# Performance work log

Hardware: AMD Instinct MI355X
Metric: run time of the kernel (lower is better)

Reference implementation:

```python
import jax, jax.numpy as jnp
import numpy as np

B, W, H, C = 8, 32, 32, 64   # batch, width, height, hidden_size
NH = 8                        # num_attention_heads
M = 32                        # max_position_embeddings
P = C // 2                    # position_embedding_size (query_positional_score=True)


def setup_inputs() -> dict:
    key = jax.random.key(0)
    ks = jax.random.split(key, 7)
    s = 0.02
    return {
        "hidden_states": jax.random.normal(ks[0], (B, W, H, C), dtype=jnp.float32),
        "row_emb": jax.random.normal(ks[1], (2 * M - 1, P), dtype=jnp.float32) * s,
        "col_emb": jax.random.normal(ks[2], (2 * M - 1, P), dtype=jnp.float32) * s,
        "Wq": jax.random.normal(ks[3], (NH * C, C), dtype=jnp.float32) * s,
        "bq": jnp.zeros((NH * C,), dtype=jnp.float32),
        "Wk": jax.random.normal(ks[4], (NH * C, C), dtype=jnp.float32) * s,
        "bk": jnp.zeros((NH * C,), dtype=jnp.float32),
        "Wv": jax.random.normal(ks[5], (C, NH * C), dtype=jnp.float32) * s,
        "bv": jnp.zeros((C,), dtype=jnp.float32),
    }


def reference(hidden_states, row_emb, col_emb, Wq, bq, Wk, bk, Wv, bv):
    b, w, h, c = hidden_states.shape
    nh = Wq.shape[0] // c
    half = c // 2
    center = row_emb.shape[0] // 2  # = max_position_embeddings - 1

    # projections: all_head_size = nh * c (per source: hidden_size * num_heads)
    q = (hidden_states @ Wq.T + bq).reshape(b, w, h, nh, c)
    k = (hidden_states @ Wk.T + bk).reshape(b, w, h, nh, c)

    # relative index tables: rel[i, j] = (j - i) + (M - 1)
    iw = jnp.arange(w)
    ih = jnp.arange(h)
    rel_w = iw[None, :] - iw[:, None] + center   # (w, w)
    rel_h = ih[None, :] - ih[:, None] + center   # (h, h)
    r_emb = row_emb[rel_w]  # (w, w, P)
    c_emb = col_emb[rel_h]  # (h, h, P)

    # positional scores: q split into row/col halves
    q_row = q[..., :half]
    q_col = q[..., half:]
    row_scores = jnp.einsum('bijhd,ikd->bijhk', q_row, r_emb)  # (b,w,h,nh,w)
    col_scores = jnp.einsum('bijhd,jld->bijhl', q_col, c_emb)  # (b,w,h,nh,h)
    scale = jnp.sqrt(jnp.asarray(c, dtype=hidden_states.dtype))
    scores = (row_scores[..., :, None] + col_scores[..., None, :]) / scale  # (b,w,h,nh,w,h)

    # content scores q^T k
    scores = scores + jnp.einsum('bijhd,bklhd->bijhkl', q, k) / scale

    # softmax over merged spatial key dims (k,l)
    probs = jax.nn.softmax(scores.reshape(b, w, h, nh, w * h), axis=-1).reshape(scores.shape)

    # value mixing directly with hidden_states, then output projection
    mixed = jnp.einsum('bijhkl,bkld->bijhd', probs, hidden_states).reshape(b, w, h, nh * c)
    return mixed @ Wv.T + bv
```

## Files before the change

### kernel.cpp

```cpp
#include <hip/hip_runtime.h>
#include <math.h>

typedef __bf16 bf16;
typedef bf16 bf16x2 __attribute__((ext_vector_type(2)));
typedef bf16 bf16x4 __attribute__((ext_vector_type(4)));
typedef bf16 bf16x8 __attribute__((ext_vector_type(8)));
typedef float f32x4 __attribute__((ext_vector_type(4)));

constexpr int CENTER = 31;
constexpr float QSCALE = 0.125f * 1.4426950408889634f;

static __device__ __forceinline__ unsigned short f2bf_bits(float f) {
    bf16 b = (bf16)f;
    return __builtin_bit_cast(unsigned short, b);
}

static __device__ __forceinline__ float fast_exp2(float x) {
#if __has_builtin(__builtin_amdgcn_exp2f)
    return __builtin_amdgcn_exp2f(x);
#else
    return exp2f(x);
#endif
}

__global__ __launch_bounds__(256)
void prep_kernel(const float* __restrict__ hid,
                 const float* __restrict__ Wq, const float* __restrict__ Wk,
                 const float* __restrict__ Wv,
                 bf16* __restrict__ hb, bf16* __restrict__ htb,
                 bf16* __restrict__ Wqb, bf16* __restrict__ Wkb,
                 bf16* __restrict__ Wvp)
{
    __shared__ __attribute__((aligned(16))) bf16 hs[64][72];

    const int t   = threadIdx.x;
    const int blk = blockIdx.x;
    const int b   = blk >> 4, kc = blk & 15;

    {
        int row = t >> 2, c4 = (t & 3) * 16;
        const float4* src = (const float4*)(hid + ((size_t)b * 1024 + kc * 64 + row) * 64 + c4);
        bf16 tmp[16];
        #pragma unroll
        for (int u = 0; u < 4; ++u) {
            float4 v = src[u];
            tmp[4*u+0] = (bf16)v.x; tmp[4*u+1] = (bf16)v.y;
            tmp[4*u+2] = (bf16)v.z; tmp[4*u+3] = (bf16)v.w;
        }
        *(int4*)&hs[row][c4]     = ((int4*)tmp)[0];
        *(int4*)&hs[row][c4 + 8] = ((int4*)tmp)[1];
        bf16* hdst = hb + ((size_t)b * 1024 + kc * 64 + row) * 64 + c4;
        *(int4*)hdst       = ((int4*)tmp)[0];
        *(int4*)(hdst + 8) = ((int4*)tmp)[1];
    }

    {
        int idx = blk * 256 + t;
        if (idx < 8192) {
            float4 vq = ((const float4*)Wq)[idx];
            float4 vk = ((const float4*)Wk)[idx];
            float4 vv = ((const float4*)Wv)[idx];
            ushort4 pq, pk2, pv;
            pq.x = f2bf_bits(vq.x); pq.y = f2bf_bits(vq.y); pq.z = f2bf_bits(vq.z); pq.w = f2bf_bits(vq.w);
            pk2.x = f2bf_bits(vk.x); pk2.y = f2bf_bits(vk.y); pk2.z = f2bf_bits(vk.z); pk2.w = f2bf_bits(vk.w);
            pv.x = f2bf_bits(vv.x); pv.y = f2bf_bits(vv.y); pv.z = f2bf_bits(vv.z); pv.w = f2bf_bits(vv.w);
            ((ushort4*)Wqb)[idx] = pq;
            ((ushort4*)Wkb)[idx] = pk2;
            int c = idx >> 7, o4 = (idx & 127) * 4;
            size_t dst = (size_t)((c >> 4) * 16 + (o4 >> 5)) * 512 + (c & 15) * 32 + (o4 & 31);
            *(ushort4*)(Wvp + dst) = pv;
        }
    }
    __syncthreads();

    {
        int d = t >> 2, p0 = (t & 3) * 16;
        ushort tmp[16];
        #pragma unroll
        for (int i = 0; i < 16; ++i)
            tmp[i] = __builtin_bit_cast(unsigned short, hs[p0 + i][d]);
        bf16* dst = htb + ((size_t)b * 64 + d) * 1024 + kc * 64 + p0;
        *(int4*)dst       = ((int4*)tmp)[0];
        *(int4*)(dst + 8) = ((int4*)tmp)[1];
    }
}

__global__ __launch_bounds__(256)
void qkproj_kernel(const bf16* __restrict__ hb,
                   const bf16* __restrict__ Wqb, const float* __restrict__ bq,
                   const bf16* __restrict__ Wkb, const float* __restrict__ bk,
                   bf16* __restrict__ qb, bf16* __restrict__ kb)
{
    __shared__ __attribute__((aligned(16))) bf16 As[128][72];
    __shared__ __attribute__((aligned(16))) bf16 Bs[128][72];

    const int t  = threadIdx.x;
    const int pt = blockIdx.x;
    const int ot = blockIdx.y;
    const int z  = blockIdx.z;
    const int p0 = pt * 128;
    const int b  = p0 >> 10;

    const bf16* Wb        = z ? Wkb : Wqb;
    const float* bias     = z ? bk : bq;
    bf16* outp            = z ? kb : qb;
    const float scale     = z ? 1.0f : QSCALE;

    {
        int row = t >> 1, ch = (t & 1) * 32;
        const int4* asrc = (const int4*)(hb + (size_t)(p0 + row) * 64 + ch);
        const int4* bsrc = (const int4*)(Wb + (size_t)(ot * 128 + row) * 64 + ch);
        #pragma unroll
        for (int u = 0; u < 4; ++u) {
            *(int4*)&As[row][ch + u * 8] = asrc[u];
            *(int4*)&Bs[row][ch + u * 8] = bsrc[u];
        }
    }
    __syncthreads();

    const int w = t >> 6, ln = t & 63, l15 = ln & 15, quad = ln >> 4;

    bf16x8 a[2][2];
    #pragma unroll
    for (int mt = 0; mt < 2; ++mt) {
        a[mt][0] = *(const bf16x8*)&As[w * 32 + mt * 16 + l15][quad * 8];
        a[mt][1] = *(const bf16x8*)&As[w * 32 + mt * 16 + l15][32 + quad * 8];
    }

    const f32x4 z4 = {0.f, 0.f, 0.f, 0.f};
    f32x4 acc[2][8];
    #pragma unroll
    for (int mt = 0; mt < 2; ++mt)
        #pragma unroll
        for (int nt = 0; nt < 8; ++nt) acc[mt][nt] = z4;

    #pragma unroll
    for (int nt = 0; nt < 8; ++nt) {
        bf16x8 b0 = *(const bf16x8*)&Bs[nt * 16 + l15][quad * 8];
        bf16x8 b1 = *(const bf16x8*)&Bs[nt * 16 + l15][32 + quad * 8];
        #pragma unroll
        for (int mt = 0; mt < 2; ++mt) {
            acc[mt][nt] = __builtin_amdgcn_mfma_f32_16x16x32_bf16(a[mt][0], b0, acc[mt][nt], 0, 0, 0);
            acc[mt][nt] = __builtin_amdgcn_mfma_f32_16x16x32_bf16(a[mt][1], b1, acc[mt][nt], 0, 0, 0);
        }
    }

    #pragma unroll
    for (int nt = 0; nt < 8; ++nt) {
        int o = ot * 128 + nt * 16 + l15;
        float bv = bias[o];
        int hh = o >> 6, d = o & 63;
        #pragma unroll
        for (int mt = 0; mt < 2; ++mt)
            #pragma unroll
            for (int r = 0; r < 4; ++r) {
                int pos = (p0 & 1023) + w * 32 + mt * 16 + quad * 4 + r;
                float val = (acc[mt][nt][r] + bv) * scale;
                outp[(((size_t)b * 8 + hh) * 1024 + pos) * 64 + d] = (bf16)val;
            }
    }
}

__global__ __launch_bounds__(256)
void bias_kernel(const bf16* __restrict__ qb,
                 const float* __restrict__ row_emb, const float* __restrict__ col_emb,
                 bf16* __restrict__ rowbias, bf16* __restrict__ colbias)
{
    __shared__ __attribute__((aligned(16))) bf16 embRs[63][40];
    __shared__ __attribute__((aligned(16))) bf16 embCs[63][40];

    const int t  = threadIdx.x;
    const int bh = blockIdx.x;
    const int sg = blockIdx.y;

    for (int i = t; i < 2016; i += 256) embRs[i >> 5][i & 31] = (bf16)row_emb[i];
    for (int i = t; i < 2016; i += 256) embCs[i >> 5][i & 31] = (bf16)col_emb[i];
    __syncthreads();

    const int w = t >> 6, ln = t & 63, l15 = ln & 15, quad = ln >> 4;

    #pragma unroll
    for (int u = 0; u < 2; ++u) {
        int s = sg * 8 + u * 4 + w;
        bool cm = s >= 32;
        int ij = cm ? s - 32 : s;

        bf16x8 a[2];
        #pragma unroll
        for (int mt = 0; mt < 2; ++mt) {
            const bf16* ap = cm
                ? qb + ((size_t)bh * 1024 + (mt * 16 + l15) * 32 + ij) * 64 + 32 + quad * 8
                : qb + ((size_t)bh * 1024 + ij * 32 + mt * 16 + l15) * 64 + quad * 8;
            a[mt] = *(const bf16x8*)ap;
        }
        bf16* ob = cm ? colbias : rowbias;

        #pragma unroll
        for (int nt = 0; nt < 2; ++nt) {
            int erow = nt * 16 + l15 + CENTER - ij;
            bf16x8 bfrag = cm ? *(const bf16x8*)&embCs[erow][quad * 8]
                              : *(const bf16x8*)&embRs[erow][quad * 8];
            #pragma unroll
            for (int mt = 0; mt < 2; ++mt) {
                f32x4 c = {0.f, 0.f, 0.f, 0.f};
                c = __builtin_amdgcn_mfma_f32_16x16x32_bf16(a[mt], bfrag, c, 0, 0, 0);
                #pragma unroll
                for (int r = 0; r < 4; ++r) {
                    int ql = mt * 16 + quad * 4 + r;
                    int qrow = cm ? ql * 32 + ij : ij * 32 + ql;
                    ob[((size_t)bh * 1024 + qrow) * 32 + nt * 16 + l15] = (bf16)c[r];
                }
            }
        }
    }
}

__global__ __launch_bounds__(256, 2)
void attn_kernel(const bf16* __restrict__ qb, const bf16* __restrict__ kb,
                 const bf16* __restrict__ htb,
                 const bf16* __restrict__ rowbias, const bf16* __restrict__ colbias,
                 bf16* __restrict__ mixedb)
{
    __shared__ __attribute__((aligned(16))) bf16 Ks[64][72];
    __shared__ __attribute__((aligned(16))) bf16 Hts[64][72];
    __shared__ __attribute__((aligned(16))) bf16 Pp[4][32][72];

    const int t  = threadIdx.x;
    const int id = blockIdx.x;
    const int r8 = id & 7;
    const int g  = id >> 3;
    const int qt = g & 7;
    const int bh = r8 * 8 + (g >> 3);
    const int b  = bh >> 3, h = bh & 7;
    const int q0 = qt * 128;
    const int w = t >> 6, ln = t & 63, l15 = ln & 15, quad = ln >> 4;

    bf16x8 bq_[2][2];
    float  cbv[2][2][4];
    const bf16* rbp[2];
    #pragma unroll
    for (int mt = 0; mt < 2; ++mt) {
        int qrow = q0 + w * 32 + mt * 16 + l15;
        const bf16* qp = qb + ((size_t)bh * 1024 + qrow) * 64;
        bq_[mt][0] = *(const bf16x8*)(qp + quad * 8);
        bq_[mt][1] = *(const bf16x8*)(qp + 32 + quad * 8);
        #pragma unroll
        for (int par = 0; par < 2; ++par) {
            bf16x4 cv = *(const bf16x4*)(colbias + ((size_t)bh * 1024 + qrow) * 32 + par * 16 + quad * 4);
            #pragma unroll
            for (int r = 0; r < 4; ++r) cbv[mt][par][r] = (float)cv[r];
        }
        rbp[mt] = rowbias + ((size_t)bh * 1024 + qrow) * 32;
    }

    const f32x4 z4 = {0.f, 0.f, 0.f, 0.f};
    f32x4 oacc[2][4];
    float lsum[2] = {0.f, 0.f};
    #pragma unroll
    for (int mt = 0; mt < 2; ++mt)
        #pragma unroll
        for (int dt = 0; dt < 4; ++dt) oacc[mt][dt] = z4;

    bf16* Pw = &Pp[w][0][0];
    const bf16* kcbase = kb + (size_t)bh * 1024 * 64;
    const bf16* hcbase = htb + (size_t)b * 64 * 1024;

    const int srow = t >> 2, sc = (t & 3) << 4;
    const bf16* kptr = kcbase + (size_t)srow * 64 + sc;
    const bf16* hptr = hcbase + (size_t)srow * 1024 + sc;

    int4 kr0 = *(const int4*)(kptr);
    int4 kr1 = *(const int4*)(kptr + 8);
    int4 hr0 = *(const int4*)(hptr);
    int4 hr1 = *(const int4*)(hptr + 8);
    bf16x2 rnext[2];
    #pragma unroll
    for (int mt = 0; mt < 2; ++mt) rnext[mt] = *(const bf16x2*)(rbp[mt]);

    for (int kc = 0; kc < 16; ++kc) {
        __syncthreads();
        *(int4*)&Ks[srow][sc]      = kr0;
        *(int4*)&Ks[srow][sc + 8]  = kr1;
        *(int4*)&Hts[srow][sc]     = hr0;
        *(int4*)&Hts[srow][sc + 8] = hr1;
        float rb[2][2];
        #pragma unroll
        for (int mt = 0; mt < 2; ++mt) {
            rb[mt][0] = (float)rnext[mt][0];
            rb[mt][1] = (float)rnext[mt][1];
        }
        __syncthreads();

        if (kc < 15) {
            const bf16* kn = kptr + (size_t)(kc + 1) * 4096;
            const bf16* hn = hptr + (size_t)(kc + 1) * 64;
            kr0 = *(const int4*)(kn);
            kr1 = *(const int4*)(kn + 8);
            hr0 = *(const int4*)(hn);
            hr1 = *(const int4*)(hn + 8);
            #pragma unroll
            for (int mt = 0; mt < 2; ++mt)
                rnext[mt] = *(const bf16x2*)(rbp[mt] + (kc + 1) * 2);
        }

        f32x4 sf[2][4];
        #pragma unroll
        for (int mt = 0; mt < 2; ++mt)
            #pragma unroll
            for (int kt = 0; kt < 4; ++kt) sf[mt][kt] = z4;
        __builtin_amdgcn_s_setprio(1);
        #pragma unroll
        for (int kt = 0; kt < 4; ++kt) {
            bf16x8 aK0 = *(const bf16x8*)&Ks[kt * 16 + l15][quad * 8];
            bf16x8 aK1 = *(const bf16x8*)&Ks[kt * 16 + l15][32 + quad * 8];
            #pragma unroll
            for (int mt = 0; mt < 2; ++mt) {
                sf[mt][kt] = __builtin_amdgcn_mfma_f32_16x16x32_bf16(aK0, bq_[mt][0], sf[mt][kt], 0, 0, 0);
                sf[mt][kt] = __builtin_amdgcn_mfma_f32_16x16x32_bf16(aK1, bq_[mt][1], sf[mt][kt], 0, 0, 0);
            }
        }
        __builtin_amdgcn_s_setprio(0);

        #pragma unroll
        for (int mt = 0; mt < 2; ++mt)
            #pragma unroll
            for (int kt = 0; kt < 4; ++kt) {
                float rbv = rb[mt][kt >> 1];
                ushort4 pk;
                float p0 = fast_exp2(sf[mt][kt][0] + rbv + cbv[mt][kt & 1][0]);
                float p1 = fast_exp2(sf[mt][kt][1] + rbv + cbv[mt][kt & 1][1]);
                float p2 = fast_exp2(sf[mt][kt][2] + rbv + cbv[mt][kt & 1][2]);
                float p3 = fast_exp2(sf[mt][kt][3] + rbv + cbv[mt][kt & 1][3]);
                lsum[mt] += (p0 + p1) + (p2 + p3);
                pk.x = f2bf_bits(p0); pk.y = f2bf_bits(p1);
                pk.z = f2bf_bits(p2); pk.w = f2bf_bits(p3);
                *(ushort4*)&Pw[(mt * 16 + l15) * 72 + kt * 16 + quad * 4] = pk;
            }

        bf16x8 bp[2][2];
        #pragma unroll
        for (int mt = 0; mt < 2; ++mt) {
            bp[mt][0] = *(const bf16x8*)&Pw[(mt * 16 + l15) * 72 + quad * 8];
            bp[mt][1] = *(const bf16x8*)&Pw[(mt * 16 + l15) * 72 + 32 + quad * 8];
        }
        __builtin_amdgcn_s_setprio(1);
        #pragma unroll
        for (int dt = 0; dt < 4; ++dt) {
            bf16x8 aH0 = *(const bf16x8*)&Hts[dt * 16 + l15][quad * 8];
            bf16x8 aH1 = *(const bf16x8*)&Hts[dt * 16 + l15][32 + quad * 8];
            #pragma unroll
            for (int mt = 0; mt < 2; ++mt) {
                oacc[mt][dt] = __builtin_amdgcn_mfma_f32_16x16x32_bf16(aH0, bp[mt][0], oacc[mt][dt], 0, 0, 0);
                oacc[mt][dt] = __builtin_amdgcn_mfma_f32_16x16x32_bf16(aH1, bp[mt][1], oacc[mt][dt], 0, 0, 0);
            }
        }
        __builtin_amdgcn_s_setprio(0);
    }

    float inv[2];
    #pragma unroll
    for (int mt = 0; mt < 2; ++mt) {
        float v = lsum[mt];
        v += __shfl_xor(v, 16);
        v += __shfl_xor(v, 32);
        inv[mt] = 1.0f / v;
    }
    #pragma unroll
    for (int mt = 0; mt < 2; ++mt) {
        int pos = q0 + w * 32 + mt * 16 + l15;
        bf16* mb = mixedb + ((size_t)b * 1024 + pos) * 512 + h * 64;
        #pragma unroll
        for (int dt = 0; dt < 4; ++dt) {
            ushort4 pk;
            pk.x = f2bf_bits(oacc[mt][dt][0] * inv[mt]);
            pk.y = f2bf_bits(oacc[mt][dt][1] * inv[mt]);
            pk.z = f2bf_bits(oacc[mt][dt][2] * inv[mt]);
            pk.w = f2bf_bits(oacc[mt][dt][3] * inv[mt]);
            *(ushort4*)(mb + dt * 16 + quad * 4) = pk;
        }
    }
}

__global__ __launch_bounds__(256)
void out_proj_kernel(const bf16* __restrict__ mixedb,
                     const bf16* __restrict__ Wvp, const float* __restrict__ bv,
                     float* __restrict__ out)
{
    const int t  = threadIdx.x;
    const int p0 = blockIdx.x * 16;
    const int w = t >> 6, ln = t & 63, l15 = ln & 15, quad = ln >> 4;

    float bvv = bv[w * 16 + l15];
    f32x4 acc = {bvv, bvv, bvv, bvv};

    const bf16* arow  = mixedb + (size_t)(p0 + l15) * 512 + quad * 8;
    const bf16* bbase = Wvp + (size_t)w * 16 * 512 + l15 * 32 + quad * 8;

    #pragma unroll
    for (int kc = 0; kc < 16; ++kc) {
        bf16x8 a0 = *(const bf16x8*)(arow + kc * 32);
        bf16x8 bfrag = *(const bf16x8*)(bbase + kc * 512);
        acc = __builtin_amdgcn_mfma_f32_16x16x32_bf16(a0, bfrag, acc, 0, 0, 0);
    }

    #pragma unroll
    for (int r = 0; r < 4; ++r)
        out[(size_t)(p0 + quad * 4 + r) * 64 + w * 16 + l15] = acc[r];
}

extern "C" void kernel_launch(void* const* d_in, const int* in_sizes, int n_in,
                              void* d_out, int out_size, void* d_ws, size_t ws_size,
                              hipStream_t stream)
{
    const float* hid     = (const float*)d_in[0];
    const float* row_emb = (const float*)d_in[1];
    const float* col_emb = (const float*)d_in[2];
    const float* Wq      = (const float*)d_in[3];
    const float* bq      = (const float*)d_in[4];
    const float* Wk      = (const float*)d_in[5];
    const float* bk      = (const float*)d_in[6];
    const float* Wv      = (const float*)d_in[7];
    const float* bv      = (const float*)d_in[8];
    float* out = (float*)d_out;

    bf16* qb      = (bf16*)d_ws;
    bf16* kb      = qb + (size_t)64 * 1024 * 64;
    bf16* htb     = kb + (size_t)64 * 1024 * 64;
    bf16* rowbias = htb + (size_t)8 * 64 * 1024;
    bf16* colbias = rowbias + (size_t)64 * 1024 * 32;
    bf16* mixedb  = colbias + (size_t)64 * 1024 * 32;
    bf16* hb      = mixedb + (size_t)8 * 1024 * 512;
    bf16* Wqb     = hb + (size_t)8 * 1024 * 64;
    bf16* Wkb     = Wqb + (size_t)512 * 64;
    bf16* Wvp     = Wkb + (size_t)512 * 64;

    prep_kernel<<<128, 256, 0, stream>>>(hid, Wq, Wk, Wv, hb, htb, Wqb, Wkb, Wvp);
    qkproj_kernel<<<dim3(64, 4, 2), 256, 0, stream>>>(hb, Wqb, bq, Wkb, bk, qb, kb);
    bias_kernel<<<dim3(64, 8), 256, 0, stream>>>(qb, row_emb, col_emb, rowbias, colbias);
    attn_kernel<<<512, 256, 0, stream>>>(qb, kb, htb, rowbias, colbias, mixedb);
    out_proj_kernel<<<512, 256, 0, stream>>>(mixedb, Wvp, bv, out);
}
```

Measured before the change: 133.3 us.

## Double-buffer K/H tiles in attention and process two row tiles per out-proj block

The attention kernel now keeps two shared-memory buffers for the K and hidden-state tiles. Global loads are prefetched two chunks ahead and the next tile is written into the spare buffer, so each iteration needs one barrier instead of two. The output projection kernel now computes 32 rows per block, reusing each weight fragment for two MFMAs, and launches half as many blocks. The attention kernel's shared memory grows, which could limit occupancy.

```diff
diff --git a/kernel.cpp b/kernel.cpp
--- a/kernel.cpp
+++ b/kernel.cpp
@@ -221,8 +221,8 @@
                  const bf16* __restrict__ rowbias, const bf16* __restrict__ colbias,
                  bf16* __restrict__ mixedb)
 {
-    __shared__ __attribute__((aligned(16))) bf16 Ks[64][72];
-    __shared__ __attribute__((aligned(16))) bf16 Hts[64][72];
+    __shared__ __attribute__((aligned(16))) bf16 Ks[2][64][72];
+    __shared__ __attribute__((aligned(16))) bf16 Hts[2][64][72];
     __shared__ __attribute__((aligned(16))) bf16 Pp[4][32][72];
 
     const int t  = threadIdx.x;
@@ -273,36 +273,49 @@
     int4 kr1 = *(const int4*)(kptr + 8);
     int4 hr0 = *(const int4*)(hptr);
     int4 hr1 = *(const int4*)(hptr + 8);
+    *(int4*)&Ks[0][srow][sc]       = kr0;
+    *(int4*)&Ks[0][srow][sc + 8]   = kr1;
+    *(int4*)&Hts[0][srow][sc]      = hr0;
+    *(int4*)&Hts[0][srow][sc + 8]  = hr1;
+    kr0 = *(const int4*)(kptr + 4096);
+    kr1 = *(const int4*)(kptr + 4096 + 8);
+    hr0 = *(const int4*)(hptr + 64);
+    hr1 = *(const int4*)(hptr + 64 + 8);
     bf16x2 rnext[2];
     #pragma unroll
     for (int mt = 0; mt < 2; ++mt) rnext[mt] = *(const bf16x2*)(rbp[mt]);
-
+    __syncthreads();
+
+    int cur = 0;
     for (int kc = 0; kc < 16; ++kc) {
-        __syncthreads();
-        *(int4*)&Ks[srow][sc]      = kr0;
-        *(int4*)&Ks[srow][sc + 8]  = kr1;
-        *(int4*)&Hts[srow][sc]     = hr0;
-        *(int4*)&Hts[srow][sc + 8] = hr1;
+        if (kc < 15) {
+            *(int4*)&Ks[cur ^ 1][srow][sc]      = kr0;
+            *(int4*)&Ks[cur ^ 1][srow][sc + 8]  = kr1;
+            *(int4*)&Hts[cur ^ 1][srow][sc]     = hr0;
+            *(int4*)&Hts[cur ^ 1][srow][sc + 8] = hr1;
+        }
         float rb[2][2];
         #pragma unroll
         for (int mt = 0; mt < 2; ++mt) {
             rb[mt][0] = (float)rnext[mt][0];
             rb[mt][1] = (float)rnext[mt][1];
         }
-        __syncthreads();
-
-        if (kc < 15) {
-            const bf16* kn = kptr + (size_t)(kc + 1) * 4096;
-            const bf16* hn = hptr + (size_t)(kc + 1) * 64;
+        if (kc < 14) {
+            const bf16* kn = kptr + (size_t)(kc + 2) * 4096;
+            const bf16* hn = hptr + (size_t)(kc + 2) * 64;
             kr0 = *(const int4*)(kn);
             kr1 = *(const int4*)(kn + 8);
             hr0 = *(const int4*)(hn);
             hr1 = *(const int4*)(hn + 8);
+        }
+        if (kc < 15) {
             #pragma unroll
             for (int mt = 0; mt < 2; ++mt)
                 rnext[mt] = *(const bf16x2*)(rbp[mt] + (kc + 1) * 2);
         }
 
+        const bf16 (* __restrict__ Kc)[72]  = Ks[cur];
+        const bf16 (* __restrict__ Hc)[72]  = Hts[cur];
         f32x4 sf[2][4];
         #pragma unroll
         for (int mt = 0; mt < 2; ++mt)
@@ -311,8 +324,8 @@
         __builtin_amdgcn_s_setprio(1);
         #pragma unroll
         for (int kt = 0; kt < 4; ++kt) {
-            bf16x8 aK0 = *(const bf16x8*)&Ks[kt * 16 + l15][quad * 8];
-            bf16x8 aK1 = *(const bf16x8*)&Ks[kt * 16 + l15][32 + quad * 8];
+            bf16x8 aK0 = *(const bf16x8*)&Kc[kt * 16 + l15][quad * 8];
+            bf16x8 aK1 = *(const bf16x8*)&Kc[kt * 16 + l15][32 + quad * 8];
             #pragma unroll
             for (int mt = 0; mt < 2; ++mt) {
                 sf[mt][kt] = __builtin_amdgcn_mfma_f32_16x16x32_bf16(aK0, bq_[mt][0], sf[mt][kt], 0, 0, 0);
@@ -346,8 +359,8 @@
         __builtin_amdgcn_s_setprio(1);
         #pragma unroll
         for (int dt = 0; dt < 4; ++dt) {
-            bf16x8 aH0 = *(const bf16x8*)&Hts[dt * 16 + l15][quad * 8];
-            bf16x8 aH1 = *(const bf16x8*)&Hts[dt * 16 + l15][32 + quad * 8];
+            bf16x8 aH0 = *(const bf16x8*)&Hc[dt * 16 + l15][quad * 8];
+            bf16x8 aH1 = *(const bf16x8*)&Hc[dt * 16 + l15][32 + quad * 8];
             #pragma unroll
             for (int mt = 0; mt < 2; ++mt) {
                 oacc[mt][dt] = __builtin_amdgcn_mfma_f32_16x16x32_bf16(aH0, bp[mt][0], oacc[mt][dt], 0, 0, 0);
@@ -355,6 +368,9 @@
             }
         }
         __builtin_amdgcn_s_setprio(0);
+
+        __syncthreads();
+        cur ^= 1;
     }
 
     float inv[2];
@@ -387,25 +403,30 @@
                      float* __restrict__ out)
 {
     const int t  = threadIdx.x;
-    const int p0 = blockIdx.x * 16;
+    const int p0 = blockIdx.x * 32;
     const int w = t >> 6, ln = t & 63, l15 = ln & 15, quad = ln >> 4;
 
     float bvv = bv[w * 16 + l15];
-    f32x4 acc = {bvv, bvv, bvv, bvv};
-
-    const bf16* arow  = mixedb + (size_t)(p0 + l15) * 512 + quad * 8;
+    f32x4 acc[2] = {(f32x4){bvv, bvv, bvv, bvv}, (f32x4){bvv, bvv, bvv, bvv}};
+
+    const bf16* arow0 = mixedb + (size_t)(p0 + l15) * 512 + quad * 8;
+    const bf16* arow1 = mixedb + (size_t)(p0 + 16 + l15) * 512 + quad * 8;
     const bf16* bbase = Wvp + (size_t)w * 16 * 512 + l15 * 32 + quad * 8;
 
     #pragma unroll
     for (int kc = 0; kc < 16; ++kc) {
-        bf16x8 a0 = *(const bf16x8*)(arow + kc * 32);
+        bf16x8 a0 = *(const bf16x8*)(arow0 + kc * 32);
+        bf16x8 a1 = *(const bf16x8*)(arow1 + kc * 32);
         bf16x8 bfrag = *(const bf16x8*)(bbase + kc * 512);
-        acc = __builtin_amdgcn_mfma_f32_16x16x32_bf16(a0, bfrag, acc, 0, 0, 0);
-    }
-
-    #pragma unroll
-    for (int r = 0; r < 4; ++r)
-        out[(size_t)(p0 + quad * 4 + r) * 64 + w * 16 + l15] = acc[r];
+        acc[0] = __builtin_amdgcn_mfma_f32_16x16x32_bf16(a0, bfrag, acc[0], 0, 0, 0);
+        acc[1] = __builtin_amdgcn_mfma_f32_16x16x32_bf16(a1, bfrag, acc[1], 0, 0, 0);
+    }
+
+    #pragma unroll
+    for (int mt = 0; mt < 2; ++mt)
+        #pragma unroll
+        for (int r = 0; r < 4; ++r)
+            out[(size_t)(p0 + mt * 16 + quad * 4 + r) * 64 + w * 16 + l15] = acc[mt][r];
 }
 
 extern "C" void kernel_launch(void* const* d_in, const int* in_sizes, int n_in,
@@ -438,5 +459,5 @@
     qkproj_kernel<<<dim3(64, 4, 2), 256, 0, stream>>>(hb, Wqb, bq, Wkb, bk, qb, kb);
     bias_kernel<<<dim3(64, 8), 256, 0, stream>>>(qb, row_emb, col_emb, rowbias, colbias);
     attn_kernel<<<512, 256, 0, stream>>>(qb, kb, htb, rowbias, colbias, mixedb);
-    out_proj_kernel<<<512, 256, 0, stream>>>(mixedb, Wvp, bv, out);
-}
+    out_proj_kernel<<<256, 256, 0, stream>>>(mixedb, Wvp, bv, out);
+}
```

Measured after the change: 131.3 us. About the same (-1.5%).
